# Kernel tuning notes

Hardware: AMD Instinct MI355X
Metric: run time of the kernel (lower is better)

The kernel has to match this reference:

```python
import jax, jax.numpy as jnp
import numpy as np

B, N, F = 16, 4096, 3

def setup_inputs() -> dict:
    key = jax.random.key(0)
    k1, k2 = jax.random.split(key)
    array1 = jax.random.normal(k1, (B, N, F), dtype=jnp.float32)
    array2 = jax.random.normal(k2, (B, N, F), dtype=jnp.float32)
    return {"array1": array1, "array2": array2}

def reference(array1, array2):
    # D[b, i, j] = ||array1[b, i] - array2[b, j]||^2, via expansion identity
    sq1 = jnp.sum(array1 * array1, axis=-1)              # [B, N1]
    sq2 = jnp.sum(array2 * array2, axis=-1)              # [B, N2]
    cross = jnp.einsum('bnd,bmd->bnm', array1, array2)   # [B, N1, N2]
    D = sq1[:, :, None] + sq2[:, None, :] - 2.0 * cross  # [B, N1, N2]
    # av_dist1: for each sample in array2, min dist to array1, then mean
    av_dist1 = jnp.mean(jnp.min(D, axis=1), axis=1)      # [B]
    # av_dist2: for each sample in array1, min dist to array2, then mean
    av_dist2 = jnp.mean(jnp.min(D, axis=2), axis=1)      # [B]
    dist = jnp.mean(0.5 * av_dist1 + 0.5 * av_dist2)
    return dist * 100.0
```

## Files before the change

kernel.cpp:

```cpp
#include <hip/hip_runtime.h>


constexpr int B_ = 16;
constexpr int N_ = 4096;
constexpr int BN = B_ * N_;
constexpr int BLK = 256;
constexpr int JT = N_ / 16;

using bf16x8 = __attribute__((ext_vector_type(8))) __bf16;
using f32x4  = __attribute__((ext_vector_type(4))) float;

__device__ inline uint bf16_rne(float f) {
    uint u = __float_as_uint(f);
    return (u + 0x7FFFu + ((u >> 16) & 1u)) >> 16;
}
__device__ inline float bf16_f(uint h) { return __uint_as_float(h << 16); }

__global__ __launch_bounds__(BLK)
void prep_kernel(const float* __restrict__ a1, const float* __restrict__ a2,
                 uint4* __restrict__ A1, uint4* __restrict__ B1,
                 uint4* __restrict__ A2, uint4* __restrict__ B2) {
    int gi = blockIdx.x * BLK + threadIdx.x;
    const float* in = blockIdx.y ? a2 : a1;
    uint4* Ao = blockIdx.y ? A2 : A1;
    uint4* Bo = blockIdx.y ? B2 : B1;
    float x = in[3 * gi], y = in[3 * gi + 1], z = in[3 * gi + 2];
    float sq = fmaf(x, x, fmaf(y, y, z * z));
    float t = -0.5f * sq;
    uint hx = bf16_rne(x), hy = bf16_rne(y), hz = bf16_rne(z);
    uint lx = bf16_rne(x - bf16_f(hx));
    uint ly = bf16_rne(y - bf16_f(hy));
    uint lz = bf16_rne(z - bf16_f(hz));
    uint th = bf16_rne(t);
    uint tl = bf16_rne(t - bf16_f(th));
    const uint ONE = 0x3F80u;
    Ao[2 * gi]     = make_uint4(hx | (hy << 16), hz | (lx << 16), ly | (lz << 16), hx | (hy << 16));
    Ao[2 * gi + 1] = make_uint4(hz | (ONE << 16), ONE | (th << 16), tl, 0u);
    Bo[2 * gi]     = make_uint4(hx | (hy << 16), hz | (hx << 16), hy | (hz << 16), lx | (ly << 16));
    Bo[2 * gi + 1] = make_uint4(lz | (th << 16), tl | (ONE << 16), ONE, 0u);
}

#define PFOLD2(Qa, Qb) {                                                         \
    f32x4 o0 = __builtin_amdgcn_mfma_f32_16x16x32_bf16(a0, (Qa), cz, 0, 0, 0);   \
    f32x4 o1 = __builtin_amdgcn_mfma_f32_16x16x32_bf16(a1, (Qa), cz, 0, 0, 0);   \
    f32x4 o2 = __builtin_amdgcn_mfma_f32_16x16x32_bf16(a0, (Qb), cz, 0, 0, 0);   \
    f32x4 o3 = __builtin_amdgcn_mfma_f32_16x16x32_bf16(a1, (Qb), cz, 0, 0, 0);   \
    _Pragma("unroll")                                                            \
    for (int r = 0; r < 4; ++r) {                                                \
        vm0[r] = fmaxf(fmaxf(vm0[r], o0[r]), o2[r]);                             \
        vm1[r] = fmaxf(fmaxf(vm1[r], o1[r]), o3[r]);                             \
    } }

__global__ __launch_bounds__(BLK, 4)
void minmax_kernel(const uint4* __restrict__ A1u, const uint4* __restrict__ B1u,
                   const uint4* __restrict__ A2u, const uint4* __restrict__ B2u,
                   float* __restrict__ bsums) {
    int d = blockIdx.z, b = blockIdx.y;
    const bf16x8* __restrict__ Aarr = (const bf16x8*)(d ? A2u : A1u);
    const bf16x8* __restrict__ Barr = (const bf16x8*)(d ? B1u : B2u);
    int tid = threadIdx.x;
    int L = tid & 63, w = tid >> 6;
    int lpt = L & 15, hi = (L >> 4) & 1;
    bool act = L < 32;
    int ibase = blockIdx.x * 128 + w * 32;

    const bf16x8* pA = Aarr + (size_t)(b * N_ + ibase + lpt) * 2 + hi;
    const bf16x8* pB = Barr + (size_t)(b * N_ + lpt) * 2 + hi;

    uint4 zu; zu.x = zu.y = zu.z = zu.w = 0u;
    bf16x8 zf = __builtin_bit_cast(bf16x8, zu);
    bf16x8 a0 = act ? pA[0] : zf;
    bf16x8 a1 = act ? pA[32] : zf;
    f32x4 cz = {0.f, 0.f, 0.f, 0.f};
    f32x4 vm0 = {-3.0e38f, -3.0e38f, -3.0e38f, -3.0e38f};
    f32x4 vm1 = vm0;

    bf16x8 p0 = pB[0], p1 = pB[32], p2 = pB[64], p3 = pB[96];
#pragma unroll 1
    for (int jt = 0; jt < JT - 4; jt += 4) {
        bf16x8 n0 = pB[(size_t)(jt + 4) * 32], n1 = pB[(size_t)(jt + 5) * 32];
        bf16x8 n2 = pB[(size_t)(jt + 6) * 32], n3 = pB[(size_t)(jt + 7) * 32];
        PFOLD2(p0, p1)
        PFOLD2(p2, p3)
        p0 = n0; p1 = n1; p2 = n2; p3 = n3;
    }
    PFOLD2(p0, p1)
    PFOLD2(p2, p3)

#pragma unroll
    for (int off = 1; off < 16; off <<= 1) {
#pragma unroll
        for (int r = 0; r < 4; ++r) {
            vm0[r] = fmaxf(vm0[r], __shfl_xor(vm0[r], off));
            vm1[r] = fmaxf(vm1[r], __shfl_xor(vm1[r], off));
        }
    }
    float v = (vm0[0] + vm0[1]) + (vm0[2] + vm0[3])
            + (vm1[0] + vm1[1]) + (vm1[2] + vm1[3]);
    v += __shfl_xor(v, 16);
    v += __shfl_xor(v, 32);

    __shared__ float red4[4];
    if (L == 0) red4[w] = v;
    __syncthreads();
    if (tid == 0) {
        int bid = blockIdx.x + 32 * blockIdx.y + 512 * blockIdx.z;
        bsums[bid] = red4[0] + red4[1] + red4[2] + red4[3];
    }
}

__global__ __launch_bounds__(BLK)
void reduce_final(const float* __restrict__ bs, float* __restrict__ out) {
    int t = threadIdx.x;
    float v = (bs[t] + bs[t + 256]) + (bs[t + 512] + bs[t + 768]);
    for (int off = 32; off; off >>= 1) v += __shfl_down(v, off, 64);
    __shared__ float red4[4];
    int lane = t & 63, w = t >> 6;
    if (lane == 0) red4[w] = v;
    __syncthreads();
    if (t == 0) out[0] = (red4[0] + red4[1] + red4[2] + red4[3]) * (-100.0f / (float)BN);
}

extern "C" void kernel_launch(void* const* d_in, const int* in_sizes, int n_in,
                              void* d_out, int out_size, void* d_ws, size_t ws_size,
                              hipStream_t stream) {
    const float* a1 = (const float*)d_in[0];
    const float* a2 = (const float*)d_in[1];
    char* ws = (char*)d_ws;
    uint4* A1 = (uint4*)(ws);
    uint4* B1 = (uint4*)(ws + (2u << 20));
    uint4* A2 = (uint4*)(ws + (4u << 20));
    uint4* B2 = (uint4*)(ws + (6u << 20));
    float* bsums = (float*)(ws + (8u << 20));
    float* out = (float*)d_out;

    prep_kernel<<<dim3(BN / BLK, 2), BLK, 0, stream>>>(a1, a2, A1, B1, A2, B2);
    minmax_kernel<<<dim3(N_ / 128, B_, 2), BLK, 0, stream>>>(A1, B1, A2, B2, bsums);
    reduce_final<<<dim3(1), BLK, 0, stream>>>(bsums, out);
}
```

Measured before the change: 45.22 us.

## Halve per-wave row tile to double block count and occupancy

Each wave now handles 16 query points with one A fragment instead of 32 with two, so the grid doubles to 2048 blocks and the launch bound asks for 8 blocks per SIMD-CU slot. The inner loop is restructured to process 8 column tiles per iteration with interleaved prefetch, and the final reduction reads 2048 partial sums. This trades B-operand reuse (each loaded B tile now feeds one MFMA instead of two, doubling B traffic) for more parallelism and latency hiding.

```diff
diff --git a/kernel.cpp b/kernel.cpp
--- a/kernel.cpp
+++ b/kernel.cpp
@@ -40,18 +40,18 @@
     Bo[2 * gi + 1] = make_uint4(lz | (th << 16), tl | (ONE << 16), ONE, 0u);
 }
 
-#define PFOLD2(Qa, Qb) {                                                         \
-    f32x4 o0 = __builtin_amdgcn_mfma_f32_16x16x32_bf16(a0, (Qa), cz, 0, 0, 0);   \
-    f32x4 o1 = __builtin_amdgcn_mfma_f32_16x16x32_bf16(a1, (Qa), cz, 0, 0, 0);   \
-    f32x4 o2 = __builtin_amdgcn_mfma_f32_16x16x32_bf16(a0, (Qb), cz, 0, 0, 0);   \
-    f32x4 o3 = __builtin_amdgcn_mfma_f32_16x16x32_bf16(a1, (Qb), cz, 0, 0, 0);   \
+#define FOLD4(Q0, Q1, Q2, Q3) {                                                  \
+    f32x4 oA = __builtin_amdgcn_mfma_f32_16x16x32_bf16(a0, (Q0), cz, 0, 0, 0);   \
+    f32x4 oB = __builtin_amdgcn_mfma_f32_16x16x32_bf16(a0, (Q1), cz, 0, 0, 0);   \
+    f32x4 oC = __builtin_amdgcn_mfma_f32_16x16x32_bf16(a0, (Q2), cz, 0, 0, 0);   \
+    f32x4 oD = __builtin_amdgcn_mfma_f32_16x16x32_bf16(a0, (Q3), cz, 0, 0, 0);   \
     _Pragma("unroll")                                                            \
     for (int r = 0; r < 4; ++r) {                                                \
-        vm0[r] = fmaxf(fmaxf(vm0[r], o0[r]), o2[r]);                             \
-        vm1[r] = fmaxf(fmaxf(vm1[r], o1[r]), o3[r]);                             \
+        vm0[r] = fmaxf(fmaxf(vm0[r], oA[r]), oB[r]);                             \
+        vm0[r] = fmaxf(fmaxf(vm0[r], oC[r]), oD[r]);                             \
     } }
 
-__global__ __launch_bounds__(BLK, 4)
+__global__ __launch_bounds__(BLK, 8)
 void minmax_kernel(const uint4* __restrict__ A1u, const uint4* __restrict__ B1u,
                    const uint4* __restrict__ A2u, const uint4* __restrict__ B2u,
                    float* __restrict__ bsums) {
@@ -62,7 +62,7 @@
     int L = tid & 63, w = tid >> 6;
     int lpt = L & 15, hi = (L >> 4) & 1;
     bool act = L < 32;
-    int ibase = blockIdx.x * 128 + w * 32;
+    int ibase = blockIdx.x * 64 + w * 16;
 
     const bf16x8* pA = Aarr + (size_t)(b * N_ + ibase + lpt) * 2 + hi;
     const bf16x8* pB = Barr + (size_t)(b * N_ + lpt) * 2 + hi;
@@ -70,33 +70,32 @@
     uint4 zu; zu.x = zu.y = zu.z = zu.w = 0u;
     bf16x8 zf = __builtin_bit_cast(bf16x8, zu);
     bf16x8 a0 = act ? pA[0] : zf;
-    bf16x8 a1 = act ? pA[32] : zf;
     f32x4 cz = {0.f, 0.f, 0.f, 0.f};
     f32x4 vm0 = {-3.0e38f, -3.0e38f, -3.0e38f, -3.0e38f};
-    f32x4 vm1 = vm0;
 
     bf16x8 p0 = pB[0], p1 = pB[32], p2 = pB[64], p3 = pB[96];
 #pragma unroll 1
-    for (int jt = 0; jt < JT - 4; jt += 4) {
-        bf16x8 n0 = pB[(size_t)(jt + 4) * 32], n1 = pB[(size_t)(jt + 5) * 32];
-        bf16x8 n2 = pB[(size_t)(jt + 6) * 32], n3 = pB[(size_t)(jt + 7) * 32];
-        PFOLD2(p0, p1)
-        PFOLD2(p2, p3)
-        p0 = n0; p1 = n1; p2 = n2; p3 = n3;
+    for (int jt = 0; jt + 8 < JT; jt += 8) {
+        const bf16x8* q = pB + (size_t)jt * 32;
+        bf16x8 n0 = q[128], n1 = q[160], n2 = q[192], n3 = q[224];
+        FOLD4(p0, p1, p2, p3)
+        p0 = q[256]; p1 = q[288]; p2 = q[320]; p3 = q[352];
+        FOLD4(n0, n1, n2, n3)
     }
-    PFOLD2(p0, p1)
-    PFOLD2(p2, p3)
+    {
+        const bf16x8* q = pB + (size_t)248 * 32;
+        bf16x8 n0 = q[128], n1 = q[160], n2 = q[192], n3 = q[224];
+        FOLD4(p0, p1, p2, p3)
+        FOLD4(n0, n1, n2, n3)
+    }
 
 #pragma unroll
-    for (int off = 1; off < 16; off <<= 1) {
+    for (int off = 1; off < 16; off <<= 1)
 #pragma unroll
-        for (int r = 0; r < 4; ++r) {
+        for (int r = 0; r < 4; ++r)
             vm0[r] = fmaxf(vm0[r], __shfl_xor(vm0[r], off));
-            vm1[r] = fmaxf(vm1[r], __shfl_xor(vm1[r], off));
-        }
-    }
-    float v = (vm0[0] + vm0[1]) + (vm0[2] + vm0[3])
-            + (vm1[0] + vm1[1]) + (vm1[2] + vm1[3]);
+
+    float v = (vm0[0] + vm0[1]) + (vm0[2] + vm0[3]);
     v += __shfl_xor(v, 16);
     v += __shfl_xor(v, 32);
 
@@ -104,7 +103,7 @@
     if (L == 0) red4[w] = v;
     __syncthreads();
     if (tid == 0) {
-        int bid = blockIdx.x + 32 * blockIdx.y + 512 * blockIdx.z;
+        int bid = blockIdx.x + 64 * blockIdx.y + 1024 * blockIdx.z;
         bsums[bid] = red4[0] + red4[1] + red4[2] + red4[3];
     }
 }
@@ -112,7 +111,9 @@
 __global__ __launch_bounds__(BLK)
 void reduce_final(const float* __restrict__ bs, float* __restrict__ out) {
     int t = threadIdx.x;
-    float v = (bs[t] + bs[t + 256]) + (bs[t + 512] + bs[t + 768]);
+    float v = 0.f;
+#pragma unroll
+    for (int k = 0; k < 8; ++k) v += bs[t + 256 * k];
     for (int off = 32; off; off >>= 1) v += __shfl_down(v, off, 64);
     __shared__ float red4[4];
     int lane = t & 63, w = t >> 6;
@@ -135,6 +136,6 @@
     float* out = (float*)d_out;
 
     prep_kernel<<<dim3(BN / BLK, 2), BLK, 0, stream>>>(a1, a2, A1, B1, A2, B2);
-    minmax_kernel<<<dim3(N_ / 128, B_, 2), BLK, 0, stream>>>(A1, B1, A2, B2, bsums);
+    minmax_kernel<<<dim3(N_ / 64, B_, 2), BLK, 0, stream>>>(A1, B1, A2, B2, bsums);
     reduce_final<<<dim3(1), BLK, 0, stream>>>(bsums, out);
 }
```

New measurement: 73.12 us. 1.62x slower.
